# Kernel optimization log

Measured on AMD Instinct MI355X. Metric: run time of the kernel, lower is better.

The kernel has to match this reference:

```python
import jax, jax.numpy as jnp
import numpy as np

DIM = 1024
H = 16
HD = DIM // H  # 64
K = 256


def setup_inputs() -> dict:
    key = jax.random.key(0)
    ks = jax.random.split(key, 8)
    x = jax.random.normal(ks[0], (4, 4096, DIM), dtype=jnp.float32)
    # torch nn.Linear weights are (out, in); y = x @ W.T
    Wq = jax.random.normal(ks[1], (DIM, DIM), dtype=jnp.float32) * (DIM ** -0.5)
    Wk = jax.random.normal(ks[2], (DIM, DIM), dtype=jnp.float32) * (DIM ** -0.5)
    Wv = jax.random.normal(ks[3], (DIM, DIM), dtype=jnp.float32) * (DIM ** -0.5)
    E = jax.random.normal(ks[4], (K, HD), dtype=jnp.float32)
    F = jax.random.normal(ks[5], (K, HD), dtype=jnp.float32)
    Wo = jax.random.normal(ks[6], (DIM, DIM), dtype=jnp.float32) * (DIM ** -0.5)
    bo = jax.random.normal(ks[7], (DIM,), dtype=jnp.float32) * 0.01
    return {"x": x, "Wq": Wq, "Wk": Wk, "Wv": Wv, "E": E, "F": F, "Wo": Wo, "bo": bo}


def reference(x, Wq, Wk, Wv, E, F, Wo, bo):
    B, N, D = x.shape
    d = HD
    q = (x @ Wq.T).reshape(B, N, H, d).transpose(0, 2, 1, 3)  # (B,H,N,d)
    k = (x @ Wk.T).reshape(B, N, H, d).transpose(0, 2, 1, 3)
    v = (x @ Wv.T).reshape(B, N, H, d).transpose(0, 2, 1, 3)
    # Faithful to source: einsum contracts over n (sequence), elementwise in d.
    k_proj = jnp.einsum('bhnd,kd->bhkd', k, E)  # (B,H,K,d)
    v_proj = jnp.einsum('bhnd,kd->bhkd', v, F)
    attn = jnp.einsum('bhnd,bhkd->bhnk', q, k_proj) / (d ** 0.5)  # (B,H,N,K)
    attn = jax.nn.softmax(attn, axis=-1)
    out = jnp.einsum('bhnk,bhkd->bhnd', attn, v_proj)
    out = out.transpose(0, 2, 1, 3).reshape(B, N, D)
    return out @ Wo.T + bo
```

## Files before the change

kernel.cpp:

```cpp
#include <hip/hip_runtime.h>

#define DIM 1024
#define BATCH 4
#define SEQ 4096
#define NH 16
#define HD 64
#define KP 256

typedef float f32x4 __attribute__((ext_vector_type(4)));
typedef _Float16 half8 __attribute__((ext_vector_type(8)));

__device__ __forceinline__ void gll16(const void* g, void* l) {
  __builtin_amdgcn_global_load_lds(
      (const __attribute__((address_space(1))) void*)g,
      (__attribute__((address_space(3))) void*)l, 16, 0, 0);
}

#define DPPF(v, ctrl)                                                        \
  __builtin_bit_cast(float, __builtin_amdgcn_mov_dpp(                        \
                                __builtin_bit_cast(int, v), ctrl, 0xF, 0xF, true))

__global__ void k_cvt(const float* __restrict__ s, _Float16* __restrict__ d) {
  int i = (blockIdx.x * 256 + threadIdx.x) * 8;
  f32x4 a = *(const f32x4*)(s + i);
  f32x4 b = *(const f32x4*)(s + i + 4);
  half8 h;
  h[0] = a[0]; h[1] = a[1]; h[2] = a[2]; h[3] = a[3];
  h[4] = b[0]; h[5] = b[1]; h[6] = b[2]; h[7] = b[3];
  *(half8*)(d + i) = h;
}

__global__ void k_cvtw(const float* __restrict__ Wq, const float* __restrict__ Wo,
                       _Float16* __restrict__ Wq_h, _Float16* __restrict__ Wo_h) {
  int bb = blockIdx.x;
  const float* s = (bb < 512) ? Wq : Wo;
  _Float16* d = (bb < 512) ? Wq_h : Wo_h;
  int i = ((bb & 511) * 256 + threadIdx.x) * 8;
  f32x4 a = *(const f32x4*)(s + i);
  f32x4 b = *(const f32x4*)(s + i + 4);
  half8 h;
  h[0] = a[0]; h[1] = a[1]; h[2] = a[2]; h[3] = a[3];
  h[4] = b[0]; h[5] = b[1]; h[6] = b[2]; h[7] = b[3];
  *(half8*)(d + i) = h;
}

__global__ void k_misc(const float* __restrict__ E, const float* __restrict__ F,
                       _Float16* __restrict__ E_h, _Float16* __restrict__ Ft,
                       float* __restrict__ xsum) {
  int bb = blockIdx.x;
  if (bb < 16) {
    xsum[bb * 256 + threadIdx.x] = 0.f;
  } else if (bb < 24) {
    int i = ((bb - 16) * 256 + threadIdx.x) * 8;
    f32x4 a = *(const f32x4*)(E + i);
    f32x4 b = *(const f32x4*)(E + i + 4);
    half8 h;
    h[0] = a[0]; h[1] = a[1]; h[2] = a[2]; h[3] = a[3];
    h[4] = b[0]; h[5] = b[1]; h[6] = b[2]; h[7] = b[3];
    *(half8*)(E_h + i) = h;
  } else {
    int i = (bb - 24) * 256 + threadIdx.x;
    int k = i >> 6, d = i & 63;
    Ft[d * KP + (k & 15) * 16 + (k >> 4)] = (_Float16)F[i];
  }
}

__global__ void k_xsum(const _Float16* __restrict__ xh, float* __restrict__ xs) {
  int c = blockIdx.x * 256 + threadIdx.x;
  int b = blockIdx.y;
  int n0 = blockIdx.z * 128;
  const _Float16* p = xh + (size_t)(b * SEQ + n0) * DIM + c;
  float s = 0.f;
  #pragma unroll 8
  for (int i = 0; i < 128; i++) s += (float)p[i * DIM];
  atomicAdd(&xs[b * DIM + c], s);
}

__global__ void k_sksv(const float* __restrict__ xs, const float* __restrict__ Wk,
                       const float* __restrict__ Wv, float* __restrict__ Sk,
                       float* __restrict__ Sv) {
  int idx = blockIdx.x * 4 + (threadIdx.x >> 6);
  int lane = threadIdx.x & 63;
  int kv = idx >> 12;
  int rem = idx & 4095;
  int b = rem >> 10, c = rem & 1023;
  const float* W = (kv ? Wv : Wk) + c * DIM;
  const float* xp = xs + b * DIM;
  float a = 0.f;
  #pragma unroll
  for (int i = 0; i < 16; i++) a += xp[lane + i * 64] * W[lane + i * 64];
  for (int off = 32; off; off >>= 1) a += __shfl_down(a, off);
  if (lane == 0) (kv ? Sv : Sk)[rem] = a;
}

template <int MODE>
__global__ __launch_bounds__(256) void k_gemm(const _Float16* __restrict__ A,
                                              const _Float16* __restrict__ Bw,
                                              void* __restrict__ Cout,
                                              const float* __restrict__ sb) {
  __shared__ _Float16 sh[2][128 * 32];
  _Float16* As = sh[0];
  _Float16* Bs = sh[1];
  const int tid = threadIdx.x;
  const int w = tid >> 6, lane = tid & 63;
  const int m0 = blockIdx.x * 128, n0 = blockIdx.y * 128;
  const int q4 = lane >> 4, mm = lane & 15;
  const int wm = w & 1, wn = w >> 1;
  f32x4 acc[4][4] = {};
  const _Float16* Ag = A + (m0 + w * 32 + (lane >> 2)) * DIM + (lane & 3) * 8;
  const _Float16* Bg = Bw + (n0 + w * 32 + (lane >> 2)) * DIM + (lane & 3) * 8;
  _Float16* AsW = As + w * 1024;
  _Float16* BsW = Bs + w * 1024;
  for (int k0 = 0; k0 < DIM; k0 += 32) {
    gll16(Ag + k0, AsW);
    gll16(Ag + k0 + 16 * DIM, AsW + 512);
    gll16(Bg + k0, BsW);
    gll16(Bg + k0 + 16 * DIM, BsW + 512);
    __syncthreads();
    half8 av[4], bv[4];
    const _Float16* Ap = As + (wm * 64 + mm) * 32 + q4 * 8;
    const _Float16* Bp = Bs + (wn * 64 + mm) * 32 + q4 * 8;
    #pragma unroll
    for (int t = 0; t < 4; t++) {
      av[t] = *(const half8*)(Ap + t * 512);
      bv[t] = *(const half8*)(Bp + t * 512);
    }
    #pragma unroll
    for (int mt = 0; mt < 4; mt++)
      #pragma unroll
      for (int nt = 0; nt < 4; nt++)
        acc[mt][nt] = __builtin_amdgcn_mfma_f32_16x16x32_f16(av[mt], bv[nt], acc[mt][nt], 0, 0, 0);
    __syncthreads();
  }
  if (MODE == 0) {
    _Float16* Lh = (_Float16*)sh;
    #pragma unroll
    for (int p = 0; p < 2; p++) {
      if (wm == p) {
        #pragma unroll
        for (int nt = 0; nt < 4; nt++) {
          int cl = wn * 64 + nt * 16 + mm;
          float s = sb[(m0 >> 12) * DIM + n0 + cl] * (0.125f * 1.44269504088896f);
          #pragma unroll
          for (int mt = 0; mt < 4; mt++) {
            int rl = mt * 16 + q4 * 4;
            #pragma unroll
            for (int r = 0; r < 4; r++)
              Lh[(rl + r) * 128 + cl] = (_Float16)(acc[mt][nt][r] * s);
          }
        }
      }
      __syncthreads();
      int row_l = tid >> 2, c0 = (tid & 3) * 32;
      _Float16* dst = (_Float16*)Cout + (size_t)(m0 + p * 64 + row_l) * DIM + n0 + c0;
      #pragma unroll
      for (int i = 0; i < 4; i++)
        *(half8*)(dst + i * 8) = *(half8*)(Lh + row_l * 128 + c0 + i * 8);
      __syncthreads();
    }
  } else {
    float* Lf = (float*)sh;
    #pragma unroll
    for (int p = 0; p < 4; p++) {
      if (wm == (p >> 1)) {
        #pragma unroll
        for (int nt = 0; nt < 4; nt++) {
          int cl = wn * 64 + nt * 16 + mm;
          float s = sb[n0 + cl];
          #pragma unroll
          for (int mti = 0; mti < 2; mti++) {
            int mt = (p & 1) * 2 + mti;
            int rl = mt * 16 + q4 * 4 - (p & 1) * 32;
            #pragma unroll
            for (int r = 0; r < 4; r++)
              Lf[(rl + r) * 128 + cl] = acc[mt][nt][r] + s;
          }
        }
      }
      __syncthreads();
      int row_l = tid >> 3, c0 = (tid & 7) * 16;
      float* dst = (float*)Cout + (size_t)(m0 + p * 32 + row_l) * DIM + n0 + c0;
      #pragma unroll
      for (int i = 0; i < 4; i++)
        *(f32x4*)(dst + i * 4) = *(f32x4*)(Lf + row_l * 128 + c0 + i * 4);
      __syncthreads();
    }
  }
}

__global__ __launch_bounds__(256) void k_attn(const _Float16* __restrict__ Q,
                                              const _Float16* __restrict__ E,
                                              const _Float16* __restrict__ Ftp,
                                              const float* __restrict__ Sv,
                                              _Float16* __restrict__ O) {
  __shared__ _Float16 Ps[4][16][264];
  const int tid = threadIdx.x;
  const int w = tid >> 6, lane = tid & 63;
  const int q4 = lane >> 4, mm = lane & 15;
  const int bh = blockIdx.y;
  const int b = bh >> 4, h = bh & 15;
  const int row_base = blockIdx.x * 512 + w * 128;

  half8 ef[16][2];
  #pragma unroll
  for (int t = 0; t < 16; t++)
    #pragma unroll
    for (int kk = 0; kk < 2; kk++)
      ef[t][kk] = *(const half8*)(E + (t * 16 + mm) * HD + kk * 32 + q4 * 8);
  half8 ff[4][8];
  #pragma unroll
  for (int nt = 0; nt < 4; nt++)
    #pragma unroll
    for (int kk = 0; kk < 8; kk++)
      ff[nt][kk] = *(const half8*)(Ftp + (nt * 16 + mm) * KP + kk * 32 + q4 * 8);
  float sv[4];
  #pragma unroll
  for (int nt = 0; nt < 4; nt++) sv[nt] = Sv[b * DIM + h * HD + nt * 16 + mm];

  const _Float16* Qbase = Q + ((size_t)(b * SEQ + row_base + mm)) * DIM + h * HD + q4 * 8;
  half8 qa0 = *(const half8*)(Qbase);
  half8 qa1 = *(const half8*)(Qbase + 32);

  for (int tile = 0; tile < 8; tile++) {
    f32x4 acc[16] = {};
    #pragma unroll
    for (int t = 0; t < 16; t++)
      acc[t] = __builtin_amdgcn_mfma_f32_16x16x32_f16(qa0, ef[t][0], acc[t], 0, 0, 0);
    #pragma unroll
    for (int t = 0; t < 16; t++)
      acc[t] = __builtin_amdgcn_mfma_f32_16x16x32_f16(qa1, ef[t][1], acc[t], 0, 0, 0);
    half8 qn0, qn1;
    if (tile < 7) {
      const _Float16* Qn = Qbase + (size_t)(tile + 1) * 16 * DIM;
      qn0 = *(const half8*)(Qn);
      qn1 = *(const half8*)(Qn + 32);
    }
    float mx[4] = {-1e30f, -1e30f, -1e30f, -1e30f};
    #pragma unroll
    for (int t = 0; t < 16; t++)
      #pragma unroll
      for (int r = 0; r < 4; r++) mx[r] = fmaxf(mx[r], acc[t][r]);
    #pragma unroll
    for (int r = 0; r < 4; r++) {
      float m = mx[r];
      m = fmaxf(m, DPPF(m, 0x121));
      m = fmaxf(m, DPPF(m, 0x122));
      m = fmaxf(m, DPPF(m, 0x124));
      m = fmaxf(m, DPPF(m, 0x128));
      mx[r] = m;
    }
    float sm[4] = {0.f, 0.f, 0.f, 0.f};
    #pragma unroll
    for (int t = 0; t < 16; t++)
      #pragma unroll
      for (int r = 0; r < 4; r++) {
        float p = __builtin_amdgcn_exp2f(acc[t][r] - mx[r]);
        acc[t][r] = p;
        sm[r] += p;
      }
    #pragma unroll
    for (int r = 0; r < 4; r++) {
      float s = sm[r];
      s += DPPF(s, 0x121);
      s += DPPF(s, 0x122);
      s += DPPF(s, 0x124);
      s += DPPF(s, 0x128);
      sm[r] = 1.f / s;
    }
    #pragma unroll
    for (int r = 0; r < 4; r++) {
      half8 h0, h1;
      #pragma unroll
      for (int t = 0; t < 8; t++) h0[t] = (_Float16)acc[t][r];
      #pragma unroll
      for (int t = 0; t < 8; t++) h1[t] = (_Float16)acc[t + 8][r];
      *(half8*)&Ps[w][q4 * 4 + r][mm * 16] = h0;
      *(half8*)&Ps[w][q4 * 4 + r][mm * 16 + 8] = h1;
    }
    f32x4 acc2[4] = {};
    #pragma unroll
    for (int kk = 0; kk < 8; kk++) {
      half8 pa = *(const half8*)&Ps[w][mm][kk * 32 + q4 * 8];
      #pragma unroll
      for (int nt = 0; nt < 4; nt++)
        acc2[nt] = __builtin_amdgcn_mfma_f32_16x16x32_f16(pa, ff[nt][kk], acc2[nt], 0, 0, 0);
    }
    const int rw0 = row_base + tile * 16;
    #pragma unroll
    for (int nt = 0; nt < 4; nt++)
      #pragma unroll
      for (int r = 0; r < 4; r++)
        O[(size_t)(b * SEQ + rw0 + q4 * 4 + r) * DIM + h * HD + nt * 16 + mm] =
            (_Float16)(acc2[nt][r] * (sm[r] * sv[nt]));
    qa0 = qn0;
    qa1 = qn1;
  }
}

extern "C" void kernel_launch(void* const* d_in, const int* in_sizes, int n_in,
                              void* d_out, int out_size, void* d_ws, size_t ws_size,
                              hipStream_t stream) {
  (void)in_sizes; (void)n_in; (void)out_size; (void)ws_size;
  const float* x  = (const float*)d_in[0];
  const float* Wq = (const float*)d_in[1];
  const float* Wk = (const float*)d_in[2];
  const float* Wv = (const float*)d_in[3];
  const float* E  = (const float*)d_in[4];
  const float* F  = (const float*)d_in[5];
  const float* Wo = (const float*)d_in[6];
  const float* bo = (const float*)d_in[7];
  char* ws = (char*)d_ws;
  _Float16* x_h  = (_Float16*)(ws);
  _Float16* O_h  = (_Float16*)(ws);
  _Float16* Q_h  = (_Float16*)(ws + 33554432);
  _Float16* Wq_h = (_Float16*)(ws + 67108864);
  _Float16* Wo_h = (_Float16*)(ws + 69206016);
  _Float16* E_h  = (_Float16*)(ws + 71303168);
  _Float16* Ft_h = (_Float16*)(ws + 71335936);
  float* xsum    = (float*)(ws + 71368704);
  float* Sk      = (float*)(ws + 71385088);
  float* Sv      = (float*)(ws + 71401472);
  float* out     = (float*)d_out;

  k_cvt<<<8192, 256, 0, stream>>>(x, x_h);
  k_misc<<<88, 256, 0, stream>>>(E, F, E_h, Ft_h, xsum);
  k_cvtw<<<1024, 256, 0, stream>>>(Wq, Wo, Wq_h, Wo_h);
  k_xsum<<<dim3(4, BATCH, 32), 256, 0, stream>>>(x_h, xsum);
  k_sksv<<<2048, 256, 0, stream>>>(xsum, Wk, Wv, Sk, Sv);
  k_gemm<0><<<dim3(128, 8), 256, 0, stream>>>(x_h, Wq_h, (void*)Q_h, Sk);
  k_attn<<<dim3(8, 64), 256, 0, stream>>>(Q_h, E_h, Ft_h, Sv, O_h);
  k_gemm<1><<<dim3(128, 8), 256, 0, stream>>>(O_h, Wo_h, (void*)out, bo);
}
```

Before: 314.1 us.

## Double-buffer GEMM LDS tiles, XOR-swizzle loads, and pad epilogue staging rows

The fp16 MFMA GEMM now keeps two LDS stages, so the global_load_lds prefetch of the next K tile is issued while the current tile is being multiplied. This drops one barrier per iteration and hides global latency. Tile chunks are XOR-swizzled on the store side and un-swizzled on the read side to cut LDS bank conflicts in the half8 fragment reads. The epilogue staging row strides are padded to 136 halves and 132 floats to cut bank conflicts in the transposed writes. The cost is twice the LDS for the main loop, which may lower occupancy.

```diff
diff --git a/kernel.cpp b/kernel.cpp
--- a/kernel.cpp
+++ b/kernel.cpp
@@ -98,32 +98,45 @@
                                               const _Float16* __restrict__ Bw,
                                               void* __restrict__ Cout,
                                               const float* __restrict__ sb) {
-  __shared__ _Float16 sh[2][128 * 32];
-  _Float16* As = sh[0];
-  _Float16* Bs = sh[1];
+  __shared__ _Float16 sh[2][2][128 * 32];
   const int tid = threadIdx.x;
   const int w = tid >> 6, lane = tid & 63;
-  const int m0 = blockIdx.x * 128, n0 = blockIdx.y * 128;
   const int q4 = lane >> 4, mm = lane & 15;
   const int wm = w & 1, wn = w >> 1;
+  const int m0 = blockIdx.x * 128, n0 = blockIdx.y * 128;
   f32x4 acc[4][4] = {};
-  const _Float16* Ag = A + (m0 + w * 32 + (lane >> 2)) * DIM + (lane & 3) * 8;
-  const _Float16* Bg = Bw + (n0 + w * 32 + (lane >> 2)) * DIM + (lane & 3) * 8;
-  _Float16* AsW = As + w * 1024;
-  _Float16* BsW = Bs + w * 1024;
-  for (int k0 = 0; k0 < DIM; k0 += 32) {
-    gll16(Ag + k0, AsW);
-    gll16(Ag + k0 + 16 * DIM, AsW + 512);
-    gll16(Bg + k0, BsW);
-    gll16(Bg + k0 + 16 * DIM, BsW + 512);
-    __syncthreads();
+  const int swz_st = ((lane & 3) ^ ((lane >> 3) & 3)) * 8;
+  const _Float16* Ag = A + (size_t)(m0 + w * 32 + (lane >> 2)) * DIM + swz_st;
+  const _Float16* Bg = Bw + (size_t)(n0 + w * 32 + (lane >> 2)) * DIM + swz_st;
+  const int woff = w * 1024;
+  const int rd_sw = (q4 ^ ((mm >> 1) & 3)) * 8;
+  const int rdo_a = (wm * 64 + mm) * 32 + rd_sw;
+  const int rdo_b = (wn * 64 + mm) * 32 + rd_sw;
+
+  gll16(Ag, sh[0][0] + woff);
+  gll16(Ag + 16 * DIM, sh[0][0] + woff + 512);
+  gll16(Bg, sh[0][1] + woff);
+  gll16(Bg + 16 * DIM, sh[0][1] + woff + 512);
+  __syncthreads();
+  #pragma unroll 2
+  for (int t = 0; t < 32; t++) {
+    const int cur = t & 1;
+    if (t < 31) {
+      const int k0 = (t + 1) * 32;
+      _Float16* AsW = sh[cur ^ 1][0] + woff;
+      _Float16* BsW = sh[cur ^ 1][1] + woff;
+      gll16(Ag + k0, AsW);
+      gll16(Ag + k0 + 16 * DIM, AsW + 512);
+      gll16(Bg + k0, BsW);
+      gll16(Bg + k0 + 16 * DIM, BsW + 512);
+    }
     half8 av[4], bv[4];
-    const _Float16* Ap = As + (wm * 64 + mm) * 32 + q4 * 8;
-    const _Float16* Bp = Bs + (wn * 64 + mm) * 32 + q4 * 8;
-    #pragma unroll
-    for (int t = 0; t < 4; t++) {
-      av[t] = *(const half8*)(Ap + t * 512);
-      bv[t] = *(const half8*)(Bp + t * 512);
+    const _Float16* Ap = sh[cur][0] + rdo_a;
+    const _Float16* Bp = sh[cur][1] + rdo_b;
+    #pragma unroll
+    for (int i = 0; i < 4; i++) {
+      av[i] = *(const half8*)(Ap + i * 512);
+      bv[i] = *(const half8*)(Bp + i * 512);
     }
     #pragma unroll
     for (int mt = 0; mt < 4; mt++)
@@ -146,7 +159,7 @@
             int rl = mt * 16 + q4 * 4;
             #pragma unroll
             for (int r = 0; r < 4; r++)
-              Lh[(rl + r) * 128 + cl] = (_Float16)(acc[mt][nt][r] * s);
+              Lh[(rl + r) * 136 + cl] = (_Float16)(acc[mt][nt][r] * s);
           }
         }
       }
@@ -155,7 +168,7 @@
       _Float16* dst = (_Float16*)Cout + (size_t)(m0 + p * 64 + row_l) * DIM + n0 + c0;
       #pragma unroll
       for (int i = 0; i < 4; i++)
-        *(half8*)(dst + i * 8) = *(half8*)(Lh + row_l * 128 + c0 + i * 8);
+        *(half8*)(dst + i * 8) = *(half8*)(Lh + row_l * 136 + c0 + i * 8);
       __syncthreads();
     }
   } else {
@@ -173,7 +186,7 @@
             int rl = mt * 16 + q4 * 4 - (p & 1) * 32;
             #pragma unroll
             for (int r = 0; r < 4; r++)
-              Lf[(rl + r) * 128 + cl] = acc[mt][nt][r] + s;
+              Lf[(rl + r) * 132 + cl] = acc[mt][nt][r] + s;
           }
         }
       }
@@ -182,7 +195,7 @@
       float* dst = (float*)Cout + (size_t)(m0 + p * 32 + row_l) * DIM + n0 + c0;
       #pragma unroll
       for (int i = 0; i < 4; i++)
-        *(f32x4*)(dst + i * 4) = *(f32x4*)(Lf + row_l * 128 + c0 + i * 4);
+        *(f32x4*)(dst + i * 4) = *(f32x4*)(Lf + row_l * 132 + c0 + i * 4);
       __syncthreads();
     }
   }
```

New measurement: 308.7 us. No clear change (-1.7%).

## Rewrite fp16 GEMM with 256x256 tiles, 4-stage LDS pipeline and swizzle

Applied to the files above, without the earlier changes.

The projection GEMMs move from 128x128 tiles with 256 threads to 256x256 tiles with 512 threads. They use a four-buffer LDS ring that prefetches two k-steps ahead, an XOR swizzle on the LDS layout to avoid bank conflicts, and raised priority during MFMA bursts. The aim is to hide global-load latency, raise data reuse per tile, and cut LDS conflicts, so the two GEMMs become more compute-bound. The cost is a larger LDS footprint (128KB per block) and fewer blocks (256) to spread across the CUs. The hand-placed waitcnt and barrier logic also carries some correctness risk.

```diff
diff --git a/kernel.cpp b/kernel.cpp
--- a/kernel.cpp
+++ b/kernel.cpp
@@ -94,95 +94,143 @@
 }
 
 template <int MODE>
-__global__ __launch_bounds__(256) void k_gemm(const _Float16* __restrict__ A,
-                                              const _Float16* __restrict__ Bw,
-                                              void* __restrict__ Cout,
-                                              const float* __restrict__ sb) {
-  __shared__ _Float16 sh[2][128 * 32];
-  _Float16* As = sh[0];
-  _Float16* Bs = sh[1];
+__global__ __launch_bounds__(512, 2) void k_gemm(const _Float16* __restrict__ A,
+                                                 const _Float16* __restrict__ Bw,
+                                                 void* __restrict__ Cout,
+                                                 const float* __restrict__ sb) {
+  __shared__ _Float16 sh[4][2][8192];
   const int tid = threadIdx.x;
-  const int w = tid >> 6, lane = tid & 63;
-  const int m0 = blockIdx.x * 128, n0 = blockIdx.y * 128;
-  const int q4 = lane >> 4, mm = lane & 15;
+  const int w = tid >> 6, l = tid & 63;
+  const int q4 = l >> 4, mm = l & 15;
   const int wm = w & 1, wn = w >> 1;
-  f32x4 acc[4][4] = {};
-  const _Float16* Ag = A + (m0 + w * 32 + (lane >> 2)) * DIM + (lane & 3) * 8;
-  const _Float16* Bg = Bw + (n0 + w * 32 + (lane >> 2)) * DIM + (lane & 3) * 8;
-  _Float16* AsW = As + w * 1024;
-  _Float16* BsW = Bs + w * 1024;
-  for (int k0 = 0; k0 < DIM; k0 += 32) {
-    gll16(Ag + k0, AsW);
-    gll16(Ag + k0 + 16 * DIM, AsW + 512);
-    gll16(Bg + k0, BsW);
-    gll16(Bg + k0 + 16 * DIM, BsW + 512);
-    __syncthreads();
-    half8 av[4], bv[4];
-    const _Float16* Ap = As + (wm * 64 + mm) * 32 + q4 * 8;
-    const _Float16* Bp = Bs + (wn * 64 + mm) * 32 + q4 * 8;
-    #pragma unroll
-    for (int t = 0; t < 4; t++) {
-      av[t] = *(const half8*)(Ap + t * 512);
-      bv[t] = *(const half8*)(Bp + t * 512);
-    }
-    #pragma unroll
-    for (int mt = 0; mt < 4; mt++)
-      #pragma unroll
-      for (int nt = 0; nt < 4; nt++)
-        acc[mt][nt] = __builtin_amdgcn_mfma_f32_16x16x32_f16(av[mt], bv[nt], acc[mt][nt], 0, 0, 0);
-    __syncthreads();
+  const int m0 = blockIdx.x * 256, n0 = blockIdx.y * 256;
+  f32x4 acc[8][4] = {};
+
+  const int schunk = ((l & 3) ^ ((l >> 3) & 3)) * 8;
+  const _Float16* Ag = A + (size_t)(m0 + w * 32 + (l >> 2)) * DIM + schunk;
+  const _Float16* Bg = Bw + (size_t)(n0 + w * 32 + (l >> 2)) * DIM + schunk;
+  const int sdst = w * 1024;
+  const int csw = (q4 ^ ((mm >> 1) & 3)) * 8;
+  const int rdo_a = (wm * 128 + mm) * 32 + csw;
+  const int rdo_b = (wn * 64 + mm) * 32 + csw;
+
+  gll16(Ag, &sh[0][0][sdst]);
+  gll16(Ag + 16 * DIM, &sh[0][0][sdst + 512]);
+  gll16(Bg, &sh[0][1][sdst]);
+  gll16(Bg + 16 * DIM, &sh[0][1][sdst + 512]);
+  gll16(Ag + 32, &sh[1][0][sdst]);
+  gll16(Ag + 32 + 16 * DIM, &sh[1][0][sdst + 512]);
+  gll16(Bg + 32, &sh[1][1][sdst]);
+  gll16(Bg + 32 + 16 * DIM, &sh[1][1][sdst + 512]);
+  asm volatile("s_waitcnt vmcnt(4)" ::: "memory");
+  __builtin_amdgcn_s_barrier();
+
+  for (int o4 = 0; o4 < 32; o4 += 4) {
+    #pragma unroll
+    for (int s = 0; s < 4; s++) {
+      const int t = o4 + s;
+      const int rs = (s + 2) & 3;
+      const _Float16* Ap = &sh[s][0][rdo_a];
+      const _Float16* Bp = &sh[s][1][rdo_b];
+      const int kn = (t + 2) * 32;
+      half8 av[4], bv[4];
+      #pragma unroll
+      for (int i = 0; i < 4; i++) av[i] = *(const half8*)(Ap + i * 512);
+      #pragma unroll
+      for (int i = 0; i < 4; i++) bv[i] = *(const half8*)(Bp + i * 512);
+      if (t < 30) {
+        gll16(Ag + kn, &sh[rs][0][sdst]);
+        gll16(Ag + kn + 16 * DIM, &sh[rs][0][sdst + 512]);
+      }
+      __builtin_amdgcn_s_barrier();
+      asm volatile("s_waitcnt lgkmcnt(0)" ::: "memory");
+      __builtin_amdgcn_sched_barrier(0);
+      __builtin_amdgcn_s_setprio(1);
+      #pragma unroll
+      for (int mt = 0; mt < 4; mt++)
+        #pragma unroll
+        for (int nt = 0; nt < 4; nt++)
+          acc[mt][nt] = __builtin_amdgcn_mfma_f32_16x16x32_f16(av[mt], bv[nt], acc[mt][nt], 0, 0, 0);
+      __builtin_amdgcn_s_setprio(0);
+      __builtin_amdgcn_s_barrier();
+      #pragma unroll
+      for (int i = 0; i < 4; i++) av[i] = *(const half8*)(Ap + 2048 + i * 512);
+      if (t < 30) {
+        gll16(Bg + kn, &sh[rs][1][sdst]);
+        gll16(Bg + kn + 16 * DIM, &sh[rs][1][sdst + 512]);
+      }
+      __builtin_amdgcn_s_barrier();
+      asm volatile("s_waitcnt lgkmcnt(0)" ::: "memory");
+      __builtin_amdgcn_sched_barrier(0);
+      __builtin_amdgcn_s_setprio(1);
+      #pragma unroll
+      for (int mt = 0; mt < 4; mt++)
+        #pragma unroll
+        for (int nt = 0; nt < 4; nt++)
+          acc[mt + 4][nt] = __builtin_amdgcn_mfma_f32_16x16x32_f16(av[mt], bv[nt], acc[mt + 4][nt], 0, 0, 0);
+      __builtin_amdgcn_s_setprio(0);
+      if (t < 30) {
+        asm volatile("s_waitcnt vmcnt(4)" ::: "memory");
+      } else if (t == 30) {
+        asm volatile("s_waitcnt vmcnt(0)" ::: "memory");
+      }
+      __builtin_amdgcn_s_barrier();
+    }
   }
+
   if (MODE == 0) {
     _Float16* Lh = (_Float16*)sh;
-    #pragma unroll
-    for (int p = 0; p < 2; p++) {
-      if (wm == p) {
-        #pragma unroll
-        for (int nt = 0; nt < 4; nt++) {
-          int cl = wn * 64 + nt * 16 + mm;
-          float s = sb[(m0 >> 12) * DIM + n0 + cl] * (0.125f * 1.44269504088896f);
-          #pragma unroll
-          for (int mt = 0; mt < 4; mt++) {
-            int rl = mt * 16 + q4 * 4;
-            #pragma unroll
-            for (int r = 0; r < 4; r++)
-              Lh[(rl + r) * 128 + cl] = (_Float16)(acc[mt][nt][r] * s);
-          }
-        }
-      }
-      __syncthreads();
-      int row_l = tid >> 2, c0 = (tid & 3) * 32;
-      _Float16* dst = (_Float16*)Cout + (size_t)(m0 + p * 64 + row_l) * DIM + n0 + c0;
-      #pragma unroll
-      for (int i = 0; i < 4; i++)
-        *(half8*)(dst + i * 8) = *(half8*)(Lh + row_l * 128 + c0 + i * 8);
-      __syncthreads();
-    }
-  } else {
-    float* Lf = (float*)sh;
+    const float lsc = 0.125f * 1.44269504088896f;
     #pragma unroll
     for (int p = 0; p < 4; p++) {
       if (wm == (p >> 1)) {
         #pragma unroll
         for (int nt = 0; nt < 4; nt++) {
-          int cl = wn * 64 + nt * 16 + mm;
-          float s = sb[n0 + cl];
+          const int cl = wn * 64 + nt * 16 + mm;
+          const float s = sb[(m0 >> 12) * DIM + n0 + cl] * lsc;
           #pragma unroll
-          for (int mti = 0; mti < 2; mti++) {
-            int mt = (p & 1) * 2 + mti;
-            int rl = mt * 16 + q4 * 4 - (p & 1) * 32;
+          for (int mtl = 0; mtl < 4; mtl++) {
+            const int mt = (p & 1) * 4 + mtl;
+            const int rl = mtl * 16 + q4 * 4;
             #pragma unroll
             for (int r = 0; r < 4; r++)
-              Lf[(rl + r) * 128 + cl] = acc[mt][nt][r] + s;
+              Lh[(rl + r) * 264 + cl] = (_Float16)(acc[mt][nt][r] * s);
           }
         }
       }
       __syncthreads();
-      int row_l = tid >> 3, c0 = (tid & 7) * 16;
+      const int row_l = tid >> 3, c0 = (tid & 7) * 32;
+      _Float16* dst = (_Float16*)Cout + (size_t)(m0 + p * 64 + row_l) * DIM + n0 + c0;
+      #pragma unroll
+      for (int i = 0; i < 4; i++)
+        *(half8*)(dst + i * 8) = *(half8*)(Lh + row_l * 264 + c0 + i * 8);
+      __syncthreads();
+    }
+  } else {
+    float* Lf = (float*)sh;
+    #pragma unroll
+    for (int p = 0; p < 8; p++) {
+      if (wm == (p >> 2)) {
+        #pragma unroll
+        for (int nt = 0; nt < 4; nt++) {
+          const int cl = wn * 64 + nt * 16 + mm;
+          const float s = sb[n0 + cl];
+          #pragma unroll
+          for (int mtl = 0; mtl < 2; mtl++) {
+            const int mt = (p & 3) * 2 + mtl;
+            const int rl = mtl * 16 + q4 * 4;
+            #pragma unroll
+            for (int r = 0; r < 4; r++)
+              Lf[(rl + r) * 260 + cl] = acc[mt][nt][r] + s;
+          }
+        }
+      }
+      __syncthreads();
+      const int row_l = tid >> 4, c0 = (tid & 15) * 16;
       float* dst = (float*)Cout + (size_t)(m0 + p * 32 + row_l) * DIM + n0 + c0;
       #pragma unroll
       for (int i = 0; i < 4; i++)
-        *(f32x4*)(dst + i * 4) = *(f32x4*)(Lf + row_l * 128 + c0 + i * 4);
+        *(f32x4*)(dst + i * 4) = *(f32x4*)(Lf + row_l * 260 + c0 + i * 4);
       __syncthreads();
     }
   }
@@ -327,7 +375,7 @@
   k_cvtw<<<1024, 256, 0, stream>>>(Wq, Wo, Wq_h, Wo_h);
   k_xsum<<<dim3(4, BATCH, 32), 256, 0, stream>>>(x_h, xsum);
   k_sksv<<<2048, 256, 0, stream>>>(xsum, Wk, Wv, Sk, Sv);
-  k_gemm<0><<<dim3(128, 8), 256, 0, stream>>>(x_h, Wq_h, (void*)Q_h, Sk);
+  k_gemm<0><<<dim3(64, 4), 512, 0, stream>>>(x_h, Wq_h, (void*)Q_h, Sk);
   k_attn<<<dim3(8, 64), 256, 0, stream>>>(Q_h, E_h, Ft_h, Sv, O_h);
-  k_gemm<1><<<dim3(128, 8), 256, 0, stream>>>(O_h, Wo_h, (void*)out, bo);
-}
+  k_gemm<1><<<dim3(64, 4), 512, 0, stream>>>(O_h, Wo_h, (void*)out, bo);
+}
```

Result: faster. 294.2 us (-6.4%).
